# Optimization experiments

Hardware: AMD Instinct MI355X
Metric: run time of the kernel (lower is better)

## Reference

```python
import jax, jax.numpy as jnp
import numpy as np

DIM = 1024
N_HEADS = 16
HEAD_DIM = DIM // N_HEADS


def setup_inputs() -> dict:
    key = jax.random.key(0)
    k_x, k_qkv, k_out = jax.random.split(key, 3)
    B, T = 4, 2048
    x = jax.random.normal(k_x, (B, T, DIM), dtype=jnp.float32)
    W_qkv = jax.random.normal(k_qkv, (DIM, 3 * DIM), dtype=jnp.float32) * 0.02
    b_qkv = jnp.zeros((3 * DIM,), dtype=jnp.float32)
    W_out = jax.random.normal(k_out, (DIM, DIM), dtype=jnp.float32) * 0.02
    b_out = jnp.zeros((DIM,), dtype=jnp.float32)
    return {"x": x, "W_qkv": W_qkv, "b_qkv": b_qkv, "W_out": W_out, "b_out": b_out}


def reference(x, W_qkv, b_qkv, W_out, b_out):
    B, T, C = x.shape
    qkv = x @ W_qkv + b_qkv  # (B, T, 3C)
    q, k, v = jnp.split(qkv, 3, axis=-1)
    # (B, H, T, D)
    q = q.reshape(B, T, N_HEADS, HEAD_DIM).transpose(0, 2, 1, 3)
    k = k.reshape(B, T, N_HEADS, HEAD_DIM).transpose(0, 2, 1, 3)
    v = v.reshape(B, T, N_HEADS, HEAD_DIM).transpose(0, 2, 1, 3)
    scale = 1.0 / jnp.sqrt(jnp.asarray(HEAD_DIM, dtype=x.dtype))
    scores = jnp.einsum('bhqd,bhkd->bhqk', q, k) * scale  # (B, H, T, T)
    causal = jnp.tril(jnp.ones((T, T), dtype=bool))  # True = allowed
    scores = jnp.where(causal, scores, jnp.asarray(-jnp.inf, dtype=scores.dtype))
    attn = jax.nn.softmax(scores, axis=-1)
    out = jnp.einsum('bhqk,bhkd->bhqd', attn, v)  # (B, H, T, D)
    out = out.transpose(0, 2, 1, 3).reshape(B, T, C)
    return out @ W_out + b_out
```

## Files before the change

kernel.cpp:

```cpp
#include <hip/hip_runtime.h>
#include <hip/hip_bf16.h>
#include <cstdint>
#include <cstddef>

#define DIM   1024
#define NH    16
#define HD    64
#define BB    4
#define TT    2048

typedef __attribute__((ext_vector_type(8))) short bf16x8;
typedef __attribute__((ext_vector_type(4))) short bf16x4;
typedef __attribute__((ext_vector_type(4))) float f32x4;
typedef __attribute__((ext_vector_type(4))) unsigned short u16x4;
typedef unsigned short u16;
typedef unsigned int u32;

#define NEG_INF (-__builtin_inff())
#define QSCALE 0.18033688011110543f
#define AS1 __attribute__((address_space(1)))
#define AS3 __attribute__((address_space(3)))

static __device__ __forceinline__ u16 f2bf(float f) {
  union { float f; unsigned u; } v; v.f = f;
  return (u16)((v.u + 0x7FFFu + ((v.u >> 16) & 1u)) >> 16);
}

static __device__ __forceinline__ u16 bfbits(float a) {
  union { __hip_bfloat16 h; u16 u; } c; c.h = __float2bfloat16(a); return c.u;
}
static __device__ __forceinline__ u32 pk_bf16(float a, float b) {
  return (u32)bfbits(a) | ((u32)bfbits(b) << 16);
}

static __device__ __forceinline__ float exp2_fast(float x) {
  float r;
  asm("v_exp_f32 %0, %1" : "=v"(r) : "v"(x));
  return r;
}

static __device__ __forceinline__ bf16x4 tr16(u32 byte_addr) {
  bf16x4 d;
  asm volatile("ds_read_b64_tr_b16 %0, %1" : "=v"(d) : "v"(byte_addr));
  return d;
}

#define MFMA16(A, B, C) __builtin_amdgcn_mfma_f32_16x16x32_bf16(A, B, C, 0, 0, 0)
#define BARRIER asm volatile("s_barrier" ::: "memory")

__global__ __launch_bounds__(256) void k_cvt(const float* __restrict__ in,
                                             u16* __restrict__ out, int n4) {
  int i = blockIdx.x * 256 + threadIdx.x;
  if (i >= n4) return;
  float4 v = reinterpret_cast<const float4*>(in)[i];
  u16x4 o = { f2bf(v.x), f2bf(v.y), f2bf(v.z), f2bf(v.w) };
  *reinterpret_cast<u16x4*>(out + (size_t)i * 4) = o;
}

__global__ __launch_bounds__(256) void k_transpose(const float* __restrict__ in,
                                                   u16* __restrict__ out,
                                                   int R, int C) {
  __shared__ float tile[32][33];
  int bx = blockIdx.x * 32;
  int by = blockIdx.y * 32;
  int tx = threadIdx.x & 31, ty = threadIdx.x >> 5;
  #pragma unroll
  for (int i = 0; i < 32; i += 8)
    tile[ty + i][tx] = in[(size_t)(by + ty + i) * C + bx + tx];
  __syncthreads();
  #pragma unroll
  for (int i = 0; i < 32; i += 8)
    out[(size_t)(bx + ty + i) * R + by + tx] = f2bf(tile[tx][ty + i]);
}

template <int OUT_BF16>
__global__ __launch_bounds__(512, 2) void k_gemm8p(const u16* __restrict__ A,
                                                   const u16* __restrict__ Bt,
                                                   const float* __restrict__ bias,
                                                   u16* __restrict__ Cb,
                                                   float* __restrict__ Cf,
                                                   int M, int N, int K,
                                                   int scale_cols, float scale,
                                                   int nbx) {
  __shared__ __align__(16) char lds[73728];

  const int tid = threadIdx.x;
  const int nwg = gridDim.x;
  const int qq = nwg >> 3, rm = nwg & 7;
  const int xcd = blockIdx.x & 7, lidx = blockIdx.x >> 3;
  const int swz = (xcd < rm ? xcd * (qq + 1) : rm * (qq + 1) + (xcd - rm) * qq) + lidx;
  const int m0 = (swz / nbx) * 256, n0 = (swz % nbx) * 128;

  const int w = tid >> 6, lane = tid & 63;
  const int g = lane >> 4, r = lane & 15;
  const int wm = w >> 1, wn = w & 1;

  f32x4 acc[4][4] = {};
  const int KT = K >> 5;

  auto stageA = [&](int t) {
    char* base = lds + (t % 3) * 16384;
    #pragma unroll
    for (int i = 0; i < 2; ++i) {
      int o = (tid + i * 512) * 16;
      int l = o ^ (((o >> 9) & 1) << 5);
      int row = l >> 6, kb = l & 63;
      const u16* gp = A + (size_t)(m0 + row) * K + t * 32 + (kb >> 1);
      __builtin_amdgcn_global_load_lds((const AS1 void*)gp, (AS3 void*)(base + o), 16, 0, 0);
    }
  };
  auto stageB = [&](int t) {
    char* base = lds + 49152 + (t % 3) * 8192;
    int o = tid * 16;
    int l = o ^ (((o >> 9) & 1) << 5);
    int row = l >> 6, kb = l & 63;
    const u16* gp = Bt + (size_t)(n0 + row) * K + t * 32 + (kb >> 1);
    __builtin_amdgcn_global_load_lds((const AS1 void*)gp, (AS3 void*)(base + o), 16, 0, 0);
  };
  auto ldAf = [&](int t, int f) -> bf16x8 {
    const char* base = lds + (t % 3) * 16384;
    int l = (wm * 64 + f * 16 + r) * 64 + g * 16;
    return *(const bf16x8*)(base + (l ^ (((l >> 9) & 1) << 5)));
  };
  auto ldBf = [&](int t, int c) -> bf16x8 {
    const char* base = lds + 49152 + (t % 3) * 8192;
    int l = (wn * 64 + c * 16 + r) * 64 + g * 16;
    return *(const bf16x8*)(base + (l ^ (((l >> 9) & 1) << 5)));
  };

  stageA(0); stageB(0); stageA(1); stageB(1);
  asm volatile("s_waitcnt vmcnt(3)" ::: "memory");
  BARRIER;

  for (int t = 0; t < KT; ++t) {
    const bool st = (t + 2 < KT);
    bf16x8 a0 = ldAf(t, 0), a1 = ldAf(t, 1), a2 = ldAf(t, 2), a3 = ldAf(t, 3);
    bf16x8 b0 = ldBf(t, 0), b1 = ldBf(t, 1), b2 = ldBf(t, 2), b3 = ldBf(t, 3);
    if (st) { stageA(t + 2); stageB(t + 2); }
    __builtin_amdgcn_s_setprio(1);
    acc[0][0] = MFMA16(a0, b0, acc[0][0]);
    acc[0][1] = MFMA16(a0, b1, acc[0][1]);
    acc[0][2] = MFMA16(a0, b2, acc[0][2]);
    acc[0][3] = MFMA16(a0, b3, acc[0][3]);
    acc[1][0] = MFMA16(a1, b0, acc[1][0]);
    acc[1][1] = MFMA16(a1, b1, acc[1][1]);
    acc[1][2] = MFMA16(a1, b2, acc[1][2]);
    acc[1][3] = MFMA16(a1, b3, acc[1][3]);
    acc[2][0] = MFMA16(a2, b0, acc[2][0]);
    acc[2][1] = MFMA16(a2, b1, acc[2][1]);
    acc[2][2] = MFMA16(a2, b2, acc[2][2]);
    acc[2][3] = MFMA16(a2, b3, acc[2][3]);
    acc[3][0] = MFMA16(a3, b0, acc[3][0]);
    acc[3][1] = MFMA16(a3, b1, acc[3][1]);
    acc[3][2] = MFMA16(a3, b2, acc[3][2]);
    acc[3][3] = MFMA16(a3, b3, acc[3][3]);
    __builtin_amdgcn_s_setprio(0);
    if (st) asm volatile("s_waitcnt vmcnt(3)" ::: "memory");
    else    asm volatile("s_waitcnt vmcnt(0)" ::: "memory");
    BARRIER;
  }

  #pragma unroll
  for (int c = 0; c < 4; ++c) {
    int col = n0 + wn * 64 + c * 16 + r;
    float bv = bias[col];
    float sc = (col < scale_cols) ? scale : 1.0f;
    #pragma unroll
    for (int f = 0; f < 4; ++f) {
      #pragma unroll
      for (int e = 0; e < 4; ++e) {
        int row = m0 + wm * 64 + f * 16 + g * 4 + e;
        float val = (acc[f][c][e] + bv) * sc;
        if (OUT_BF16) Cb[(size_t)row * N + col] = f2bf(val);
        else          Cf[(size_t)row * N + col] = val;
      }
    }
  }
}

template <int OUT_BF16>
__global__ __launch_bounds__(256, 3) void k_gemm128(const u16* __restrict__ A,
                                                    const u16* __restrict__ Bt,
                                                    const float* __restrict__ bias,
                                                    u16* __restrict__ Cb,
                                                    float* __restrict__ Cf,
                                                    int M, int N, int K,
                                                    int scale_cols, float scale,
                                                    int nbx) {
  __shared__ __align__(16) char lds[49152];

  const int tid = threadIdx.x;
  const int nwg = gridDim.x;
  const int qq = nwg >> 3, rm = nwg & 7;
  const int xcd = blockIdx.x & 7, lidx = blockIdx.x >> 3;
  const int swz = (xcd < rm ? xcd * (qq + 1) : rm * (qq + 1) + (xcd - rm) * qq) + lidx;
  const int m0 = (swz / nbx) * 128, n0 = (swz % nbx) * 128;

  const int w = tid >> 6, lane = tid & 63;
  const int g = lane >> 4, r = lane & 15;
  const int wm = w >> 1, wn = w & 1;

  f32x4 acc[4][4] = {};
  const int KT = K >> 5;

  auto stageT = [&](char* base, const u16* src, int grow0, int kt) {
    #pragma unroll
    for (int i = 0; i < 2; ++i) {
      int o = (tid + i * 256) * 16;
      int l = o ^ (((o >> 9) & 1) << 5);
      int row = l >> 6, kb = l & 63;
      const u16* gp = src + (size_t)(grow0 + row) * K + kt * 32 + (kb >> 1);
      __builtin_amdgcn_global_load_lds((const AS1 void*)gp, (AS3 void*)(base + o), 16, 0, 0);
    }
  };
  auto stageA = [&](int t) { stageT(lds + (t % 3) * 8192, A, m0, t); };
  auto stageB = [&](int t) { stageT(lds + 24576 + (t % 3) * 8192, Bt, n0, t); };

  auto ldAf = [&](int t, int f) -> bf16x8 {
    const char* base = lds + (t % 3) * 8192;
    int l = (wm * 64 + f * 16 + r) * 64 + g * 16;
    return *(const bf16x8*)(base + (l ^ (((l >> 9) & 1) << 5)));
  };
  auto ldBf = [&](int t, int c) -> bf16x8 {
    const char* base = lds + 24576 + (t % 3) * 8192;
    int l = (wn * 64 + c * 16 + r) * 64 + g * 16;
    return *(const bf16x8*)(base + (l ^ (((l >> 9) & 1) << 5)));
  };

  stageA(0); stageB(0); stageA(1); stageB(1);
  asm volatile("s_waitcnt vmcnt(4)" ::: "memory");
  BARRIER;

  for (int t = 0; t < KT; ++t) {
    const bool st = (t + 2 < KT);
    bf16x8 a0 = ldAf(t, 0), a1 = ldAf(t, 1), a2 = ldAf(t, 2), a3 = ldAf(t, 3);
    bf16x8 b0 = ldBf(t, 0), b1 = ldBf(t, 1), b2 = ldBf(t, 2), b3 = ldBf(t, 3);
    if (st) { stageA(t + 2); stageB(t + 2); }
    __builtin_amdgcn_s_setprio(1);
    acc[0][0] = MFMA16(a0, b0, acc[0][0]);
    acc[0][1] = MFMA16(a0, b1, acc[0][1]);
    acc[0][2] = MFMA16(a0, b2, acc[0][2]);
    acc[0][3] = MFMA16(a0, b3, acc[0][3]);
    acc[1][0] = MFMA16(a1, b0, acc[1][0]);
    acc[1][1] = MFMA16(a1, b1, acc[1][1]);
    acc[1][2] = MFMA16(a1, b2, acc[1][2]);
    acc[1][3] = MFMA16(a1, b3, acc[1][3]);
    acc[2][0] = MFMA16(a2, b0, acc[2][0]);
    acc[2][1] = MFMA16(a2, b1, acc[2][1]);
    acc[2][2] = MFMA16(a2, b2, acc[2][2]);
    acc[2][3] = MFMA16(a2, b3, acc[2][3]);
    acc[3][0] = MFMA16(a3, b0, acc[3][0]);
    acc[3][1] = MFMA16(a3, b1, acc[3][1]);
    acc[3][2] = MFMA16(a3, b2, acc[3][2]);
    acc[3][3] = MFMA16(a3, b3, acc[3][3]);
    __builtin_amdgcn_s_setprio(0);
    if (st) asm volatile("s_waitcnt vmcnt(4)" ::: "memory");
    else    asm volatile("s_waitcnt vmcnt(0)" ::: "memory");
    BARRIER;
  }

  #pragma unroll
  for (int c = 0; c < 4; ++c) {
    int col = n0 + wn * 64 + c * 16 + r;
    float bv = bias[col];
    float sc = (col < scale_cols) ? scale : 1.0f;
    #pragma unroll
    for (int f = 0; f < 4; ++f) {
      #pragma unroll
      for (int e = 0; e < 4; ++e) {
        int row = m0 + wm * 64 + f * 16 + g * 4 + e;
        float val = (acc[f][c][e] + bv) * sc;
        if (OUT_BF16) Cb[(size_t)row * N + col] = f2bf(val);
        else          Cf[(size_t)row * N + col] = val;
      }
    }
  }
}

#define KVB 128
#define LBUF16 16384

__global__ __launch_bounds__(256, 2) void k_attn(const u16* __restrict__ qkv,
                                                 u16* __restrict__ aout) {
  __shared__ __align__(16) u16 smem[2 * LBUF16];

  const int bid = blockIdx.x;
  const int swz = (bid & 7) * 64 + (bid >> 3);
  const int bh = swz >> 3;
  const int p = swz & 7;
  const int b = bh >> 4, h = bh & 15;
  const int tid = threadIdx.x, w = tid >> 6, lane = tid & 63;
  const int g = lane >> 4, r = lane & 15;

  const int krow0 = tid >> 3;
  const int kcol = ((tid & 7) ^ (krow0 & 7)) * 8;
  const int vkey0 = (tid >> 1) & 63;
  const int vcol = (((tid >> 7) << 1) | (tid & 1)) * 8;
  const u16* gQ = qkv + (size_t)(b * TT) * (3 * DIM) + h * HD;
  const u16* kthr = gQ + DIM + (size_t)krow0 * (3 * DIM) + kcol;
  const u16* vthr = gQ + 2 * DIM + (size_t)vkey0 * (3 * DIM) + vcol;

  const u32 lds_base = (u32)(uintptr_t)(AS3 u16*)smem;

  auto issueKV = [&](int buf, int t) {
    u16* kb = &smem[buf * LBUF16];
    u16* vb = &smem[buf * LBUF16 + 8192];
    const size_t toff = (size_t)t * (KVB * 3 * DIM);
    const u16* kt = kthr + toff;
    const u16* vt = vthr + toff;
    #pragma unroll
    for (int i = 0; i < 4; ++i)
      __builtin_amdgcn_global_load_lds(
          (const AS1 void*)(kt + (size_t)i * 32 * 3 * DIM),
          (AS3 void*)(kb + tid * 8 + i * 2048), 16, 0, 0);
    #pragma unroll
    for (int i = 0; i < 4; ++i) {
      const u16* src = vt + (size_t)(i >> 1) * 64 * 3 * DIM + (i & 1) * 32;
      u16* dst = vb + (i >> 1) * 4096 + tid * 8 + (i & 1) * 2048;
      __builtin_amdgcn_global_load_lds((const AS1 void*)src, (AS3 void*)dst, 16, 0, 0);
    }
  };

  for (int half = 0; half < 2; ++half) {
    const int qt = half ? p : (15 - p);
    const int nt = qt + 1;
    const int qg0 = qt * 128 + w * 16 + r;

    bf16x8 qf[2][2];
    #pragma unroll
    for (int qb = 0; qb < 2; ++qb) {
      const u16* qp = gQ + (size_t)(qg0 + qb * 64) * (3 * DIM);
      #pragma unroll
      for (int kk = 0; kk < 2; ++kk)
        qf[qb][kk] = *(const bf16x8*)&qp[kk * 32 + g * 8];
    }

    f32x4 o[2][4] = {};
    float lrow[2] = { 0.f, 0.f };

    issueKV(0, 0);
    if (nt > 1) issueKV(1, 1);
    __syncthreads();

    for (int t = 0; t < nt; ++t) {
      const bool diag = (t == nt - 1);
      const u16* lk = &smem[(t & 1) * LBUF16];
      const u32 vbyte = lds_base + (t & 1) * (LBUF16 * 2) + 8192 * 2;
      const int sw = (r & 7) << 3;

      #pragma unroll
      for (int st = 0; st < 2; ++st) {
        const bool skip0 = diag && (st == 1);
        const bool m0 = diag && (st == 0);
        const bool m1 = diag && (st == 1);
        const int k0 = t * KVB + st * 64;

        bf16x8 kf[4][2];
        #pragma unroll
        for (int c = 0; c < 4; ++c) {
          const int row = st * 64 + c * 16 + r;
          kf[c][0] = *(const bf16x8*)&lk[(row * 64 + g * 8) ^ sw];
          kf[c][1] = *(const bf16x8*)&lk[(row * 64 + 32 + g * 8) ^ sw];
        }
        f32x4 s0[4] = {}, s1[4] = {};
        __builtin_amdgcn_s_setprio(1);
        #pragma unroll
        for (int c = 0; c < 4; ++c) {
          if (!skip0) {
            s0[c] = MFMA16(kf[c][0], qf[0][0], s0[c]);
            s0[c] = MFMA16(kf[c][1], qf[0][1], s0[c]);
          }
          s1[c] = MFMA16(kf[c][0], qf[1][0], s1[c]);
          s1[c] = MFMA16(kf[c][1], qf[1][1], s1[c]);
        }
        __builtin_amdgcn_s_setprio(0);

        bf16x4 tr[4][4];
        const u32 vs = vbyte + st * 8192 + (u32)lane * 8;
        #pragma unroll
        for (int cd = 0; cd < 4; ++cd)
          #pragma unroll
          for (int kh = 0; kh < 4; ++kh)
            tr[cd][kh] = tr16(vs + cd * 2048 + kh * 512);

        bf16x8 pf0[2], pf1[2];
        auto softmax = [&](f32x4* s, float& lref, bf16x8* pf, bool msk, int qg) {
          float pv[16];
          #pragma unroll
          for (int c = 0; c < 4; ++c)
            #pragma unroll
            for (int e = 0; e < 4; ++e)
              pv[c * 4 + e] = s[c][e];
          if (msk) {
            #pragma unroll
            for (int c = 0; c < 4; ++c)
              #pragma unroll
              for (int e = 0; e < 4; ++e)
                if (k0 + c * 16 + g * 4 + e > qg) pv[c * 4 + e] = NEG_INF;
          }
          #pragma unroll
          for (int i = 0; i < 16; ++i) pv[i] = exp2_fast(pv[i]);
          float a8[8];
          #pragma unroll
          for (int i = 0; i < 8; ++i) a8[i] = pv[i] + pv[i + 8];
          #pragma unroll
          for (int i = 0; i < 4; ++i) a8[i] = a8[i] + a8[i + 4];
          lref += (a8[0] + a8[1]) + (a8[2] + a8[3]);
          union { bf16x8 v; u32 wd[4]; } u0, u1;
          #pragma unroll
          for (int k = 0; k < 4; ++k) {
            u0.wd[k] = pk_bf16(pv[2 * k], pv[2 * k + 1]);
            u1.wd[k] = pk_bf16(pv[8 + 2 * k], pv[9 + 2 * k]);
          }
          pf[0] = u0.v; pf[1] = u1.v;
        };
        if (!skip0) softmax(s0, lrow[0], pf0, m0, qg0);
        softmax(s1, lrow[1], pf1, m1, qg0 + 64);

        asm volatile("s_waitcnt lgkmcnt(0)" ::: "memory");
        __builtin_amdgcn_sched_barrier(0);
        __builtin_amdgcn_s_setprio(1);
        #pragma unroll
        for (int cd = 0; cd < 4; ++cd) {
          #pragma unroll
          for (int ks = 0; ks < 2; ++ks) {
            bf16x4 lo = tr[cd][ks * 2], hi = tr[cd][ks * 2 + 1];
            bf16x8 av = { lo[0], lo[1], lo[2], lo[3], hi[0], hi[1], hi[2], hi[3] };
            if (!skip0) o[0][cd] = MFMA16(av, pf0[ks], o[0][cd]);
            o[1][cd] = MFMA16(av, pf1[ks], o[1][cd]);
          }
        }
        __builtin_amdgcn_s_setprio(0);
      }

      __syncthreads();
      if (t + 2 < nt) issueKV(t & 1, t + 2);
    }

    #pragma unroll
    for (int qb = 0; qb < 2; ++qb) {
      float l = lrow[qb];
      l += __shfl_xor(l, 16);
      l += __shfl_xor(l, 32);
      const float inv = 1.0f / l;
      u16* op = aout + (size_t)(b * TT + qg0 + qb * 64) * DIM + h * HD;
      #pragma unroll
      for (int cd = 0; cd < 4; ++cd) {
        union { u16x4 v; u32 wd[2]; } pk;
        pk.wd[0] = pk_bf16(o[qb][cd][0] * inv, o[qb][cd][1] * inv);
        pk.wd[1] = pk_bf16(o[qb][cd][2] * inv, o[qb][cd][3] * inv);
        *(u16x4*)&op[cd * 16 + g * 4] = pk.v;
      }
    }
  }
}

extern "C" void kernel_launch(void* const* d_in, const int* in_sizes, int n_in,
                              void* d_out, int out_size, void* d_ws, size_t ws_size,
                              hipStream_t stream) {
  const float* x    = (const float*)d_in[0];
  const float* Wqkv = (const float*)d_in[1];
  const float* bqkv = (const float*)d_in[2];
  const float* Wout = (const float*)d_in[3];
  const float* bout = (const float*)d_in[4];
  float* out = (float*)d_out;

  const int M = BB * TT;
  u16* xb   = (u16*)d_ws;
  u16* wqt  = xb + (size_t)M * DIM;
  u16* wot  = wqt + (size_t)3 * DIM * DIM;
  u16* qkvb = wot + (size_t)DIM * DIM;
  u16* aob  = qkvb + (size_t)M * 3 * DIM;

  k_cvt<<<(M * DIM / 4 + 255) / 256, 256, 0, stream>>>(x, xb, M * DIM / 4);
  k_transpose<<<dim3(3 * DIM / 32, DIM / 32), 256, 0, stream>>>(Wqkv, wqt, DIM, 3 * DIM);
  k_transpose<<<dim3(DIM / 32, DIM / 32), 256, 0, stream>>>(Wout, wot, DIM, DIM);

  k_gemm8p<1><<<(M / 256) * (3 * DIM / 128), 512, 0, stream>>>(
      xb, wqt, bqkv, qkvb, nullptr, M, 3 * DIM, DIM, DIM, QSCALE, 3 * DIM / 128);

  k_attn<<<BB * NH * 8, 256, 0, stream>>>(qkvb, aob);

  k_gemm128<0><<<(M / 128) * (DIM / 128), 256, 0, stream>>>(
      aob, wot, bout, nullptr, out, M, DIM, DIM, 0, 1.0f, DIM / 128);
}
```

Baseline: 153.2 us.

## Launch one attention block per query tile, heaviest first, with 64-key KV tiles

Each attention block used to handle a pair of query tiles (qt and 15-qt) so that every block did the same amount of work. Now each block handles a single 128-row query tile, the grid is doubled, and blocks are ordered so the longest causal tiles start first. The KV tile shrinks from 128 to 64 keys, which halves LDS use per block and allows finer causal masking on the last two tiles. In exchange there are twice as many loop iterations and barriers per key, and load balance now depends on the scheduler draining the uneven block sizes.

```diff
diff --git a/kernel.cpp b/kernel.cpp
--- a/kernel.cpp
+++ b/kernel.cpp
@@ -277,17 +277,17 @@
   }
 }
 
-#define KVB 128
-#define LBUF16 16384
+#define KVB 64
+#define LBUF16 8192
 
 __global__ __launch_bounds__(256, 2) void k_attn(const u16* __restrict__ qkv,
                                                  u16* __restrict__ aout) {
   __shared__ __align__(16) u16 smem[2 * LBUF16];
 
   const int bid = blockIdx.x;
-  const int swz = (bid & 7) * 64 + (bid >> 3);
-  const int bh = swz >> 3;
-  const int p = swz & 7;
+  const int xcd = bid & 7, lidx = bid >> 3;
+  const int bh = xcd * 8 + (lidx & 7);
+  const int qt = 15 - (lidx >> 3);
   const int b = bh >> 4, h = bh & 15;
   const int tid = threadIdx.x, w = tid >> 6, lane = tid & 63;
   const int g = lane >> 4, r = lane & 15;
@@ -304,153 +304,144 @@
 
   auto issueKV = [&](int buf, int t) {
     u16* kb = &smem[buf * LBUF16];
-    u16* vb = &smem[buf * LBUF16 + 8192];
+    u16* vb = &smem[buf * LBUF16 + 4096];
     const size_t toff = (size_t)t * (KVB * 3 * DIM);
     const u16* kt = kthr + toff;
     const u16* vt = vthr + toff;
     #pragma unroll
-    for (int i = 0; i < 4; ++i)
+    for (int i = 0; i < 2; ++i)
       __builtin_amdgcn_global_load_lds(
           (const AS1 void*)(kt + (size_t)i * 32 * 3 * DIM),
           (AS3 void*)(kb + tid * 8 + i * 2048), 16, 0, 0);
     #pragma unroll
-    for (int i = 0; i < 4; ++i) {
-      const u16* src = vt + (size_t)(i >> 1) * 64 * 3 * DIM + (i & 1) * 32;
-      u16* dst = vb + (i >> 1) * 4096 + tid * 8 + (i & 1) * 2048;
-      __builtin_amdgcn_global_load_lds((const AS1 void*)src, (AS3 void*)dst, 16, 0, 0);
-    }
-  };
-
-  for (int half = 0; half < 2; ++half) {
-    const int qt = half ? p : (15 - p);
-    const int nt = qt + 1;
-    const int qg0 = qt * 128 + w * 16 + r;
-
-    bf16x8 qf[2][2];
-    #pragma unroll
-    for (int qb = 0; qb < 2; ++qb) {
-      const u16* qp = gQ + (size_t)(qg0 + qb * 64) * (3 * DIM);
-      #pragma unroll
-      for (int kk = 0; kk < 2; ++kk)
-        qf[qb][kk] = *(const bf16x8*)&qp[kk * 32 + g * 8];
-    }
-
-    f32x4 o[2][4] = {};
-    float lrow[2] = { 0.f, 0.f };
-
-    issueKV(0, 0);
-    if (nt > 1) issueKV(1, 1);
+    for (int i = 0; i < 2; ++i)
+      __builtin_amdgcn_global_load_lds(
+          (const AS1 void*)(vt + i * 32),
+          (AS3 void*)(vb + tid * 8 + i * 2048), 16, 0, 0);
+  };
+
+  const int nt = 2 * qt + 2;
+  const int qg0 = qt * 128 + w * 16 + r;
+
+  bf16x8 qf[2][2];
+  #pragma unroll
+  for (int qb = 0; qb < 2; ++qb) {
+    const u16* qp = gQ + (size_t)(qg0 + qb * 64) * (3 * DIM);
+    #pragma unroll
+    for (int kk = 0; kk < 2; ++kk)
+      qf[qb][kk] = *(const bf16x8*)&qp[kk * 32 + g * 8];
+  }
+
+  f32x4 o[2][4] = {};
+  float lrow[2] = { 0.f, 0.f };
+
+  issueKV(0, 0);
+  issueKV(1, 1);
+  __syncthreads();
+
+  for (int t = 0; t < nt; ++t) {
+    const bool skip0 = (t == nt - 1);
+    const bool m0 = (t == nt - 2);
+    const bool m1 = (t == nt - 1);
+    const int k0 = t * KVB;
+    const u16* lk = &smem[(t & 1) * LBUF16];
+    const u32 vbyte = lds_base + (t & 1) * (LBUF16 * 2) + 4096 * 2;
+    const int sw = (r & 7) << 3;
+
+    bf16x8 kf[4][2];
+    #pragma unroll
+    for (int c = 0; c < 4; ++c) {
+      const int row = c * 16 + r;
+      kf[c][0] = *(const bf16x8*)&lk[(row * 64 + g * 8) ^ sw];
+      kf[c][1] = *(const bf16x8*)&lk[(row * 64 + 32 + g * 8) ^ sw];
+    }
+    f32x4 s0[4] = {}, s1[4] = {};
+    __builtin_amdgcn_s_setprio(1);
+    #pragma unroll
+    for (int c = 0; c < 4; ++c) {
+      if (!skip0) {
+        s0[c] = MFMA16(kf[c][0], qf[0][0], s0[c]);
+        s0[c] = MFMA16(kf[c][1], qf[0][1], s0[c]);
+      }
+      s1[c] = MFMA16(kf[c][0], qf[1][0], s1[c]);
+      s1[c] = MFMA16(kf[c][1], qf[1][1], s1[c]);
+    }
+    __builtin_amdgcn_s_setprio(0);
+
+    bf16x4 tr[4][4];
+    const u32 vs = vbyte + (u32)lane * 8;
+    #pragma unroll
+    for (int cd = 0; cd < 4; ++cd)
+      #pragma unroll
+      for (int kh = 0; kh < 4; ++kh)
+        tr[cd][kh] = tr16(vs + cd * 2048 + kh * 512);
+
+    bf16x8 pf0[2], pf1[2];
+    auto softmax = [&](f32x4* s, float& lref, bf16x8* pf, bool msk, int qg) {
+      float pv[16];
+      #pragma unroll
+      for (int c = 0; c < 4; ++c)
+        #pragma unroll
+        for (int e = 0; e < 4; ++e)
+          pv[c * 4 + e] = s[c][e];
+      if (msk) {
+        #pragma unroll
+        for (int c = 0; c < 4; ++c)
+          #pragma unroll
+          for (int e = 0; e < 4; ++e)
+            if (k0 + c * 16 + g * 4 + e > qg) pv[c * 4 + e] = NEG_INF;
+      }
+      #pragma unroll
+      for (int i = 0; i < 16; ++i) pv[i] = exp2_fast(pv[i]);
+      float a8[8];
+      #pragma unroll
+      for (int i = 0; i < 8; ++i) a8[i] = pv[i] + pv[i + 8];
+      #pragma unroll
+      for (int i = 0; i < 4; ++i) a8[i] = a8[i] + a8[i + 4];
+      lref += (a8[0] + a8[1]) + (a8[2] + a8[3]);
+      union { bf16x8 v; u32 wd[4]; } u0, u1;
+      #pragma unroll
+      for (int k = 0; k < 4; ++k) {
+        u0.wd[k] = pk_bf16(pv[2 * k], pv[2 * k + 1]);
+        u1.wd[k] = pk_bf16(pv[8 + 2 * k], pv[9 + 2 * k]);
+      }
+      pf[0] = u0.v; pf[1] = u1.v;
+    };
+    if (!skip0) softmax(s0, lrow[0], pf0, m0, qg0);
+    softmax(s1, lrow[1], pf1, m1, qg0 + 64);
+
+    asm volatile("s_waitcnt lgkmcnt(0)" ::: "memory");
+    __builtin_amdgcn_sched_barrier(0);
+    __builtin_amdgcn_s_setprio(1);
+    #pragma unroll
+    for (int cd = 0; cd < 4; ++cd) {
+      #pragma unroll
+      for (int ks = 0; ks < 2; ++ks) {
+        bf16x4 lo = tr[cd][ks * 2], hi = tr[cd][ks * 2 + 1];
+        bf16x8 av = { lo[0], lo[1], lo[2], lo[3], hi[0], hi[1], hi[2], hi[3] };
+        if (!skip0) o[0][cd] = MFMA16(av, pf0[ks], o[0][cd]);
+        o[1][cd] = MFMA16(av, pf1[ks], o[1][cd]);
+      }
+    }
+    __builtin_amdgcn_s_setprio(0);
+
     __syncthreads();
-
-    for (int t = 0; t < nt; ++t) {
-      const bool diag = (t == nt - 1);
-      const u16* lk = &smem[(t & 1) * LBUF16];
-      const u32 vbyte = lds_base + (t & 1) * (LBUF16 * 2) + 8192 * 2;
-      const int sw = (r & 7) << 3;
-
-      #pragma unroll
-      for (int st = 0; st < 2; ++st) {
-        const bool skip0 = diag && (st == 1);
-        const bool m0 = diag && (st == 0);
-        const bool m1 = diag && (st == 1);
-        const int k0 = t * KVB + st * 64;
-
-        bf16x8 kf[4][2];
-        #pragma unroll
-        for (int c = 0; c < 4; ++c) {
-          const int row = st * 64 + c * 16 + r;
-          kf[c][0] = *(const bf16x8*)&lk[(row * 64 + g * 8) ^ sw];
-          kf[c][1] = *(const bf16x8*)&lk[(row * 64 + 32 + g * 8) ^ sw];
-        }
-        f32x4 s0[4] = {}, s1[4] = {};
-        __builtin_amdgcn_s_setprio(1);
-        #pragma unroll
-        for (int c = 0; c < 4; ++c) {
-          if (!skip0) {
-            s0[c] = MFMA16(kf[c][0], qf[0][0], s0[c]);
-            s0[c] = MFMA16(kf[c][1], qf[0][1], s0[c]);
-          }
-          s1[c] = MFMA16(kf[c][0], qf[1][0], s1[c]);
-          s1[c] = MFMA16(kf[c][1], qf[1][1], s1[c]);
-        }
-        __builtin_amdgcn_s_setprio(0);
-
-        bf16x4 tr[4][4];
-        const u32 vs = vbyte + st * 8192 + (u32)lane * 8;
-        #pragma unroll
-        for (int cd = 0; cd < 4; ++cd)
-          #pragma unroll
-          for (int kh = 0; kh < 4; ++kh)
-            tr[cd][kh] = tr16(vs + cd * 2048 + kh * 512);
-
-        bf16x8 pf0[2], pf1[2];
-        auto softmax = [&](f32x4* s, float& lref, bf16x8* pf, bool msk, int qg) {
-          float pv[16];
-          #pragma unroll
-          for (int c = 0; c < 4; ++c)
-            #pragma unroll
-            for (int e = 0; e < 4; ++e)
-              pv[c * 4 + e] = s[c][e];
-          if (msk) {
-            #pragma unroll
-            for (int c = 0; c < 4; ++c)
-              #pragma unroll
-              for (int e = 0; e < 4; ++e)
-                if (k0 + c * 16 + g * 4 + e > qg) pv[c * 4 + e] = NEG_INF;
-          }
-          #pragma unroll
-          for (int i = 0; i < 16; ++i) pv[i] = exp2_fast(pv[i]);
-          float a8[8];
-          #pragma unroll
-          for (int i = 0; i < 8; ++i) a8[i] = pv[i] + pv[i + 8];
-          #pragma unroll
-          for (int i = 0; i < 4; ++i) a8[i] = a8[i] + a8[i + 4];
-          lref += (a8[0] + a8[1]) + (a8[2] + a8[3]);
-          union { bf16x8 v; u32 wd[4]; } u0, u1;
-          #pragma unroll
-          for (int k = 0; k < 4; ++k) {
-            u0.wd[k] = pk_bf16(pv[2 * k], pv[2 * k + 1]);
-            u1.wd[k] = pk_bf16(pv[8 + 2 * k], pv[9 + 2 * k]);
-          }
-          pf[0] = u0.v; pf[1] = u1.v;
-        };
-        if (!skip0) softmax(s0, lrow[0], pf0, m0, qg0);
-        softmax(s1, lrow[1], pf1, m1, qg0 + 64);
-
-        asm volatile("s_waitcnt lgkmcnt(0)" ::: "memory");
-        __builtin_amdgcn_sched_barrier(0);
-        __builtin_amdgcn_s_setprio(1);
-        #pragma unroll
-        for (int cd = 0; cd < 4; ++cd) {
-          #pragma unroll
-          for (int ks = 0; ks < 2; ++ks) {
-            bf16x4 lo = tr[cd][ks * 2], hi = tr[cd][ks * 2 + 1];
-            bf16x8 av = { lo[0], lo[1], lo[2], lo[3], hi[0], hi[1], hi[2], hi[3] };
-            if (!skip0) o[0][cd] = MFMA16(av, pf0[ks], o[0][cd]);
-            o[1][cd] = MFMA16(av, pf1[ks], o[1][cd]);
-          }
-        }
-        __builtin_amdgcn_s_setprio(0);
-      }
-
-      __syncthreads();
-      if (t + 2 < nt) issueKV(t & 1, t + 2);
-    }
-
-    #pragma unroll
-    for (int qb = 0; qb < 2; ++qb) {
-      float l = lrow[qb];
-      l += __shfl_xor(l, 16);
-      l += __shfl_xor(l, 32);
-      const float inv = 1.0f / l;
-      u16* op = aout + (size_t)(b * TT + qg0 + qb * 64) * DIM + h * HD;
-      #pragma unroll
-      for (int cd = 0; cd < 4; ++cd) {
-        union { u16x4 v; u32 wd[2]; } pk;
-        pk.wd[0] = pk_bf16(o[qb][cd][0] * inv, o[qb][cd][1] * inv);
-        pk.wd[1] = pk_bf16(o[qb][cd][2] * inv, o[qb][cd][3] * inv);
-        *(u16x4*)&op[cd * 16 + g * 4] = pk.v;
-      }
+    if (t + 2 < nt) issueKV(t & 1, t + 2);
+  }
+
+  #pragma unroll
+  for (int qb = 0; qb < 2; ++qb) {
+    float l = lrow[qb];
+    l += __shfl_xor(l, 16);
+    l += __shfl_xor(l, 32);
+    const float inv = 1.0f / l;
+    u16* op = aout + (size_t)(b * TT + qg0 + qb * 64) * DIM + h * HD;
+    #pragma unroll
+    for (int cd = 0; cd < 4; ++cd) {
+      union { u16x4 v; u32 wd[2]; } pk;
+      pk.wd[0] = pk_bf16(o[qb][cd][0] * inv, o[qb][cd][1] * inv);
+      pk.wd[1] = pk_bf16(o[qb][cd][2] * inv, o[qb][cd][3] * inv);
+      *(u16x4*)&op[cd * 16 + g * 4] = pk.v;
     }
   }
 }
@@ -479,7 +470,7 @@
   k_gemm8p<1><<<(M / 256) * (3 * DIM / 128), 512, 0, stream>>>(
       xb, wqt, bqkv, qkvb, nullptr, M, 3 * DIM, DIM, DIM, QSCALE, 3 * DIM / 128);
 
-  k_attn<<<BB * NH * 8, 256, 0, stream>>>(qkvb, aob);
+  k_attn<<<BB * NH * 16, 256, 0, stream>>>(qkvb, aob);
 
   k_gemm128<0><<<(M / 128) * (DIM / 128), 256, 0, stream>>>(
       aob, wot, bout, nullptr, out, M, DIM, DIM, 0, 1.0f, DIM / 128);
```

Measured after the change: 151.9 us (median of 2 runs). About the same (-0.9%).
